# Kernel tuning notes

Hardware: AMD Instinct MI355X
Metric: run time of the kernel (lower is better)

## Reference

```python
import jax, jax.numpy as jnp
import numpy as np

B, S, D, H, F = 4, 1024, 1024, 16, 4096
DH = D // H
EPS = 1e-3  # keras LayerNormalization default epsilon


def _layer_norm(x, g, b):
    mu = jnp.mean(x, axis=-1, keepdims=True)
    var = jnp.mean(jnp.square(x - mu), axis=-1, keepdims=True)
    return (x - mu) * jax.lax.rsqrt(var + EPS) * g + b


def setup_inputs() -> dict:
    key = jax.random.key(0)
    ks = jax.random.split(key, 12)
    p = lambda k, shape: (0.02 * jax.random.normal(k, shape, dtype=jnp.float32))
    inp = {
        "inputs": jax.random.normal(ks[0], (B, S, D), dtype=jnp.float32),
        "paddings": jnp.zeros((B, S), dtype=jnp.float32),
        "attention_bias": jax.random.normal(ks[1], (B, H, S, S), dtype=jnp.float32),
        "attention_mask": jnp.ones((B, S, S), dtype=jnp.float32),
        "ln1_g": jnp.ones((D,), jnp.float32), "ln1_b": jnp.zeros((D,), jnp.float32),
        "wq": p(ks[2], (D, D)), "bq": jnp.zeros((D,), jnp.float32),
        "wk": p(ks[3], (D, D)), "bk": jnp.zeros((D,), jnp.float32),
        "wv": p(ks[4], (D, D)), "bv": jnp.zeros((D,), jnp.float32),
        "wo": p(ks[5], (D, D)), "bo": jnp.zeros((D,), jnp.float32),
        "ln2_g": jnp.ones((D,), jnp.float32), "ln2_b": jnp.zeros((D,), jnp.float32),
        "w1": p(ks[6], (D, F)), "b1": jnp.zeros((F,), jnp.float32),
        "w2": p(ks[7], (F, D)), "b2": jnp.zeros((D,), jnp.float32),
    }
    return inp


def reference(inputs, paddings, attention_bias, attention_mask,
              ln1_g, ln1_b, wq, bq, wk, bk, wv, bv, wo, bo,
              ln2_g, ln2_b, w1, b1, w2, b2):
    # ----- combined mask: [B,S,S] (broadcast over heads) -----
    keep = 1.0 - paddings                           # [B,S]
    pad_mask = keep[:, :, None] * keep[:, None, :]  # [B,T,S]
    mask = attention_mask * pad_mask                # [B,T,S]

    # ----- self-attention on pre-normalized inputs -----
    xn = _layer_norm(inputs, ln1_g, ln1_b)          # [B,S,D]
    q = (xn @ wq + bq).reshape(B, S, H, DH)
    k = (xn @ wk + bk).reshape(B, S, H, DH)
    v = (xn @ wv + bv).reshape(B, S, H, DH)

    logits = jnp.einsum('bthd,bshd->bhts', q, k) / jnp.sqrt(jnp.float32(DH))
    logits = logits + attention_bias - 1e9 * (1.0 - mask[:, None, :, :])
    attn = jax.nn.softmax(logits, axis=-1)          # [B,H,T,S]
    ctx = jnp.einsum('bhts,bshd->bthd', attn, v).reshape(B, S, D)
    atten_out = ctx @ wo + bo + inputs              # residual

    # ----- feed-forward block -----
    yn = _layer_norm(atten_out, ln2_g, ln2_b)
    h = jax.nn.gelu(yn @ w1 + b1, approximate=False)  # keras 'gelu' is exact
    out = atten_out + (h @ w2 + b2)
    out = out * (1.0 - paddings[:, :, None])
    return out
```

## Files before the change

kernel.cpp:

```cpp
#include <hip/hip_runtime.h>
#include <cstdint>
#include <cstddef>

#define B_   4
#define S_   1024
#define D_   1024
#define H_   16
#define DH_  64
#define F_   4096
#define MTOT 4096
#define QKV3 3072
#define KOFF 1024
#define VOFF 2048
#define SMBASE 16.0f

typedef __bf16 bf16x8 __attribute__((ext_vector_type(8)));
typedef float  f32x4  __attribute__((ext_vector_type(4)));

__device__ __forceinline__ unsigned short f2bf(float f){
  uint32_t u = __builtin_bit_cast(uint32_t, f);
  u += 0x7fffu + ((u >> 16) & 1u);
  return (unsigned short)(u >> 16);
}

__device__ __forceinline__ void gload_lds16(const void* g, void* l){
  __builtin_amdgcn_global_load_lds((__attribute__((address_space(1))) void*)(g),
                                   (__attribute__((address_space(3))) void*)(l),
                                   16, 0, 0);
}

__global__ __launch_bounds__(256) void prep_weights(const float* __restrict__ wq,
                                                    const float* __restrict__ wk,
                                                    const float* __restrict__ wv,
                                                    const float* __restrict__ wo,
                                                    const float* __restrict__ w1,
                                                    const float* __restrict__ w2,
                                                    const float* __restrict__ bq,
                                                    const float* __restrict__ bk,
                                                    const float* __restrict__ bv,
                                                    unsigned short* __restrict__ wqkvT,
                                                    unsigned short* __restrict__ woT,
                                                    unsigned short* __restrict__ w1T,
                                                    unsigned short* __restrict__ w2T,
                                                    float* __restrict__ bqkv){
  __shared__ float tile[32][33];
  const int bid = blockIdx.x;
  const int tx = threadIdx.x, ty = threadIdx.y;
  const float* W; unsigned short* WT; int K, N, n0, k0;
  if (bid < 3072){
    W  = (bid < 1024) ? wq : (bid < 2048) ? wk : wv;
    WT = wqkvT + (size_t)(bid >> 10) * D_ * D_;
    K = D_; N = D_;
    const int t = bid & 1023; n0 = (t & 31) * 32; k0 = (t >> 5) * 32;
  } else if (bid < 4096){
    W = wo; WT = woT; K = D_; N = D_;
    const int t = bid - 3072; n0 = (t & 31) * 32; k0 = (t >> 5) * 32;
  } else if (bid < 8192){
    W = w1; WT = w1T; K = D_; N = F_;
    const int t = bid - 4096; n0 = (t & 127) * 32; k0 = (t >> 7) * 32;
  } else {
    W = w2; WT = w2T; K = F_; N = D_;
    const int t = bid - 8192; n0 = (t & 31) * 32; k0 = (t >> 5) * 32;
  }
  #pragma unroll
  for (int i = 0; i < 4; ++i)
    tile[ty + i*8][tx] = W[(size_t)(k0 + ty + i*8) * N + n0 + tx];
  __syncthreads();
  #pragma unroll
  for (int i = 0; i < 4; ++i)
    WT[(size_t)(n0 + ty + i*8) * K + k0 + tx] = f2bf(tile[tx][ty + i*8]);
  if (bid < 12){
    const int i = bid*256 + ty*32 + tx;
    bqkv[i] = (i < 1024) ? bq[i] : (i < 2048) ? bk[i - 1024] : bv[i - 2048];
  }
}

__global__ __launch_bounds__(256) void mid_prep(const unsigned short* __restrict__ qkv,
                                                unsigned short* __restrict__ vt,
                                                const float* __restrict__ amask,
                                                const float* __restrict__ pad,
                                                float* __restrict__ madd){
  const int bid = blockIdx.x;
  if (bid < 4096){
    __shared__ unsigned short tile[32][33];
    const int tx = threadIdx.x, ty = threadIdx.y;
    const int s0 = (bid & 31) * 32;
    const int d0 = ((bid >> 5) & 1) * 32;
    const int bh = bid >> 6;
    const int b = bh >> 4, hh = bh & 15;
    #pragma unroll
    for (int i = 0; i < 4; ++i)
      tile[ty + i*8][tx] = qkv[(size_t)(b*S_ + s0 + ty + i*8) * QKV3 + VOFF + hh*DH_ + d0 + tx];
    __syncthreads();
    #pragma unroll
    for (int i = 0; i < 4; ++i)
      vt[((size_t)bh*DH_ + d0 + ty + i*8) * S_ + s0 + tx] = tile[tx][ty + i*8];
  } else {
    const int tid = threadIdx.y*32 + threadIdx.x;
    const int total = B_ * S_ * S_ / 4;
    for (int idx = (bid - 4096)*256 + tid; idx < total; idx += 2048*256){
      const int e0 = idx * 4;
      const int b = e0 >> 20;
      const int t = (e0 >> 10) & (S_ - 1);
      const int s = e0 & (S_ - 1);
      const float kt = 1.0f - pad[b*S_ + t];
      const float4 m = *(const float4*)(amask + e0);
      float4 o;
      o.x = -1e9f * (1.0f - m.x * kt * (1.0f - pad[b*S_ + s + 0]));
      o.y = -1e9f * (1.0f - m.y * kt * (1.0f - pad[b*S_ + s + 1]));
      o.z = -1e9f * (1.0f - m.z * kt * (1.0f - pad[b*S_ + s + 2]));
      o.w = -1e9f * (1.0f - m.w * kt * (1.0f - pad[b*S_ + s + 3]));
      *(float4*)(madd + e0) = o;
    }
  }
}

__global__ __launch_bounds__(256) void ln_kernel(const float* __restrict__ x,
                                                 const float* __restrict__ g,
                                                 const float* __restrict__ b,
                                                 unsigned short* __restrict__ out){
  const int row = blockIdx.x;
  const int tid = threadIdx.x;
  float4 xv = ((const float4*)(x + (size_t)row * D_))[tid];
  float s  = xv.x + xv.y + xv.z + xv.w;
  float s2 = xv.x*xv.x + xv.y*xv.y + xv.z*xv.z + xv.w*xv.w;
  #pragma unroll
  for (int off = 32; off > 0; off >>= 1){
    s  += __shfl_down(s, off);
    s2 += __shfl_down(s2, off);
  }
  __shared__ float ws1[4], ws2[4];
  const int w = tid >> 6, lane = tid & 63;
  if (lane == 0){ ws1[w] = s; ws2[w] = s2; }
  __syncthreads();
  const float tot  = ws1[0] + ws1[1] + ws1[2] + ws1[3];
  const float tot2 = ws2[0] + ws2[1] + ws2[2] + ws2[3];
  const float mean = tot * (1.0f / D_);
  const float var  = tot2 * (1.0f / D_) - mean * mean;
  const float rstd = rsqrtf(var + 1e-3f);
  const int c0 = tid * 4;
  ushort4 o;
  o.x = f2bf((xv.x - mean) * rstd * g[c0+0] + b[c0+0]);
  o.y = f2bf((xv.y - mean) * rstd * g[c0+1] + b[c0+1]);
  o.z = f2bf((xv.z - mean) * rstd * g[c0+2] + b[c0+2]);
  o.w = f2bf((xv.w - mean) * rstd * g[c0+3] + b[c0+3]);
  *(ushort4*)(out + (size_t)row * D_ + c0) = o;
}

template<int EPI, int BM>
__global__ __launch_bounds__(256) void gemm_bt(const unsigned short* __restrict__ A,
                                               const unsigned short* __restrict__ BT,
                                               const float* __restrict__ bias,
                                               const float* __restrict__ resid,
                                               const float* __restrict__ pad,
                                               unsigned short* __restrict__ outB,
                                               float* __restrict__ outF,
                                               int N, int K){
  constexpr int MR = BM / 32;
  constexpr int RA = BM / 32;
  __shared__ unsigned short As[BM * 64];
  __shared__ unsigned short Bs[128 * 64];
  const int tid  = threadIdx.x;
  const int lane = tid & 63, w = tid >> 6;
  const int wr = w >> 1, wc = w & 1;
  const int lm = lane & 15, l4 = lane >> 4;
  const int xsw = (lm & 7) << 3;
  const int m0 = blockIdx.x * BM, n0 = blockIdx.y * 128;

  const int rrow = tid >> 3;
  const int ce   = (((tid & 7) ^ (rrow & 7)) << 3);
  const unsigned short* Asrc = A  + (size_t)(m0 + rrow) * K + ce;
  const unsigned short* Bsrc = BT + (size_t)(n0 + rrow) * K + ce;

  f32x4 acc[MR][4] = {};

  #pragma unroll
  for (int ra = 0; ra < RA; ++ra)
    gload_lds16(Asrc + (size_t)(ra*32) * K, &As[(ra*256 + w*64) * 8]);
  #pragma unroll
  for (int rb = 0; rb < 4; ++rb)
    gload_lds16(Bsrc + (size_t)(rb*32) * K, &Bs[(rb*256 + w*64) * 8]);

  for (int k0 = 0; k0 < K; k0 += 64){
    __syncthreads();

    bf16x8 a[MR][2], bb[4][2];
    #pragma unroll
    for (int m = 0; m < MR; ++m)
      #pragma unroll
      for (int kc = 0; kc < 2; ++kc)
        a[m][kc] = *(const bf16x8*)&As[(wr*(BM/2) + m*16 + lm)*64 + ((kc*32 + l4*8) ^ xsw)];
    #pragma unroll
    for (int n = 0; n < 4; ++n)
      #pragma unroll
      for (int kc = 0; kc < 2; ++kc)
        bb[n][kc] = *(const bf16x8*)&Bs[(wc*64 + n*16 + lm)*64 + ((kc*32 + l4*8) ^ xsw)];

    __syncthreads();

    if (k0 + 64 < K){
      #pragma unroll
      for (int ra = 0; ra < RA; ++ra)
        gload_lds16(Asrc + (size_t)(ra*32) * K + (k0 + 64), &As[(ra*256 + w*64) * 8]);
      #pragma unroll
      for (int rb = 0; rb < 4; ++rb)
        gload_lds16(Bsrc + (size_t)(rb*32) * K + (k0 + 64), &Bs[(rb*256 + w*64) * 8]);
    }

    #pragma unroll
    for (int m = 0; m < MR; ++m)
      #pragma unroll
      for (int n = 0; n < 4; ++n)
        #pragma unroll
        for (int kc = 0; kc < 2; ++kc)
          acc[m][n] = __builtin_amdgcn_mfma_f32_16x16x32_bf16(a[m][kc], bb[n][kc], acc[m][n], 0, 0, 0);
  }

  #pragma unroll
  for (int m = 0; m < MR; ++m){
    #pragma unroll
    for (int n = 0; n < 4; ++n){
      #pragma unroll
      for (int r = 0; r < 4; ++r){
        const int row = m0 + wr*(BM/2) + m*16 + l4*4 + r;
        const int col = n0 + wc*64 + n*16 + lm;
        const size_t idx = (size_t)row * N + col;
        float vv = acc[m][n][r] + bias[col];
        if constexpr (EPI == 0){
          outB[idx] = f2bf(vv);
        } else if constexpr (EPI == 1){
          outF[idx] = vv + resid[idx];
        } else if constexpr (EPI == 2){
          outB[idx] = f2bf(0.5f * vv * (1.0f + erff(vv * 0.70710678118654752f)));
        } else {
          float t = vv + resid[idx];
          outF[idx] = t * (1.0f - pad[row]);
        }
      }
    }
  }
}

__global__ __launch_bounds__(256) void attn_kernel(const unsigned short* __restrict__ qkv,
                                                   const unsigned short* __restrict__ vt,
                                                   const float* __restrict__ abias,
                                                   const float* __restrict__ madd,
                                                   unsigned short* __restrict__ ctx){
  const int bid = blockIdx.x;
  const int id2 = (bid & 7) * 128 + (bid >> 3);
  const int tt = id2 & 15, h = (id2 >> 4) & 15, b = id2 >> 8;
  const int t0 = tt * 64;
  const int tid = threadIdx.x;
  const int lane = tid & 63, w = tid >> 6;
  const int lm = lane & 15, l4 = lane >> 4;
  const int xsw = (lm & 7) << 3;

  __shared__ unsigned short Ks[64 * 64];
  __shared__ unsigned short VTs[64 * 64];
  __shared__ unsigned short Ps[4][16 * 72];

  bf16x8 aq[2];
  {
    const int tg = t0 + w*16 + lm;
    const size_t qb = (size_t)(b*S_ + tg) * QKV3 + h*DH_;
    aq[0] = *(const bf16x8*)&qkv[qb + 0  + l4*8];
    aq[1] = *(const bf16x8*)&qkv[qb + 32 + l4*8];
  }

  const unsigned short* kbase = qkv + (size_t)(b*S_) * QKV3 + KOFF + h*DH_;
  const unsigned short* vbase = vt  + (size_t)((b*H_ + h) * DH_) * S_;
  const float* biasbase = abias + (size_t)((b*H_ + h) * S_ + t0 + w*16 + l4*4) * S_;
  const float* maddbase = madd  + (size_t)(b*S_ + t0 + w*16 + l4*4) * S_;

  const int r_st  = tid >> 3;
  const int ce_st = (((tid & 7) ^ (r_st & 7)) << 3);
  const unsigned short* kst = kbase + (size_t)r_st * QKV3 + ce_st;
  const unsigned short* vst = vbase + (size_t)r_st * S_ + ce_st;

  f32x4 accO[4] = {};
  float lrow[4] = {};
  float bmA[4][4], bmB[4][4];

  #pragma unroll
  for (int n = 0; n < 4; ++n){
    const int sg = n*16 + lm;
    #pragma unroll
    for (int r = 0; r < 4; ++r)
      bmA[n][r] = biasbase[(size_t)r * S_ + sg] + maddbase[(size_t)r * S_ + sg];
  }
  gload_lds16(kst,                   &Ks[w*512]);
  gload_lds16(kst + (size_t)32*QKV3, &Ks[2048 + w*512]);
  gload_lds16(vst,                   &VTs[w*512]);
  gload_lds16(vst + 32*S_,           &VTs[2048 + w*512]);

  auto step = [&](int s0, float (&cur)[4][4], float (&nxt)[4][4]){
    __syncthreads();

    const int sn = (s0 + 64 < S_) ? (s0 + 64) : s0;
    #pragma unroll
    for (int n = 0; n < 4; ++n){
      const int sg = sn + n*16 + lm;
      #pragma unroll
      for (int r = 0; r < 4; ++r)
        nxt[n][r] = biasbase[(size_t)r * S_ + sg] + maddbase[(size_t)r * S_ + sg];
    }

    f32x4 accS[4] = {};
    __builtin_amdgcn_s_setprio(1);
    #pragma unroll
    for (int n = 0; n < 4; ++n)
      #pragma unroll
      for (int kc = 0; kc < 2; ++kc){
        bf16x8 bk_ = *(const bf16x8*)&Ks[(n*16 + lm)*64 + ((kc*32 + l4*8) ^ xsw)];
        accS[n] = __builtin_amdgcn_mfma_f32_16x16x32_bf16(aq[kc], bk_, accS[n], 0, 0, 0);
      }
    __builtin_amdgcn_s_setprio(0);

    bf16x8 bvv[4][2];
    #pragma unroll
    for (int n = 0; n < 4; ++n)
      #pragma unroll
      for (int ks = 0; ks < 2; ++ks)
        bvv[n][ks] = *(const bf16x8*)&VTs[(n*16 + lm)*64 + ((ks*32 + l4*8) ^ xsw)];

    __syncthreads();

    if (s0 + 64 < S_){
      gload_lds16(kst + (size_t)(s0 + 64)*QKV3, &Ks[w*512]);
      gload_lds16(kst + (size_t)(s0 + 96)*QKV3, &Ks[2048 + w*512]);
      gload_lds16(vst + (s0 + 64),              &VTs[w*512]);
      gload_lds16(vst + 32*S_ + (s0 + 64),      &VTs[2048 + w*512]);
    }

    float ps[4] = {};
    #pragma unroll
    for (int n = 0; n < 4; ++n){
      #pragma unroll
      for (int r = 0; r < 4; ++r){
        const float pv = __expf(fmaf(accS[n][r], 0.125f, cur[n][r]) - SMBASE);
        accS[n][r] = pv;
        ps[r] += pv;
      }
    }
    #pragma unroll
    for (int r = 0; r < 4; ++r){
      float s = ps[r];
      s += __shfl_xor(s, 1); s += __shfl_xor(s, 2);
      s += __shfl_xor(s, 4); s += __shfl_xor(s, 8);
      lrow[r] += s;
    }

    #pragma unroll
    for (int n = 0; n < 4; ++n)
      #pragma unroll
      for (int r = 0; r < 4; ++r)
        Ps[w][(l4*4 + r)*72 + n*16 + lm] = f2bf(accS[n][r]);

    __builtin_amdgcn_s_setprio(1);
    #pragma unroll
    for (int ks = 0; ks < 2; ++ks){
      bf16x8 ap = *(const bf16x8*)&Ps[w][lm*72 + ks*32 + l4*8];
      #pragma unroll
      for (int n = 0; n < 4; ++n)
        accO[n] = __builtin_amdgcn_mfma_f32_16x16x32_bf16(ap, bvv[n][ks], accO[n], 0, 0, 0);
    }
    __builtin_amdgcn_s_setprio(0);
  };

  #pragma unroll 1
  for (int s0 = 0; s0 < S_; s0 += 128){
    step(s0,      bmA, bmB);
    step(s0 + 64, bmB, bmA);
  }

  #pragma unroll
  for (int n = 0; n < 4; ++n)
    #pragma unroll
    for (int r = 0; r < 4; ++r){
      const int tg = t0 + w*16 + l4*4 + r;
      ctx[(size_t)(b*S_ + tg) * D_ + h*DH_ + n*16 + lm] = f2bf(accO[n][r] / lrow[r]);
    }
}

extern "C" void kernel_launch(void* const* d_in, const int* in_sizes, int n_in,
                              void* d_out, int out_size, void* d_ws, size_t ws_size,
                              hipStream_t stream){
  (void)in_sizes; (void)n_in; (void)out_size; (void)ws_size;
  const float* x     = (const float*)d_in[0];
  const float* pad   = (const float*)d_in[1];
  const float* abias = (const float*)d_in[2];
  const float* amask = (const float*)d_in[3];
  const float* ln1g  = (const float*)d_in[4];
  const float* ln1b  = (const float*)d_in[5];
  const float* wq    = (const float*)d_in[6];
  const float* bq    = (const float*)d_in[7];
  const float* wk    = (const float*)d_in[8];
  const float* bk    = (const float*)d_in[9];
  const float* wv    = (const float*)d_in[10];
  const float* bv    = (const float*)d_in[11];
  const float* wo    = (const float*)d_in[12];
  const float* bo    = (const float*)d_in[13];
  const float* ln2g  = (const float*)d_in[14];
  const float* ln2b  = (const float*)d_in[15];
  const float* w1    = (const float*)d_in[16];
  const float* b1    = (const float*)d_in[17];
  const float* w2    = (const float*)d_in[18];
  const float* b2    = (const float*)d_in[19];
  float* out = (float*)d_out;

  char* p = (char*)d_ws;
  auto take = [&](size_t bytes){ void* r = (void*)p; p += bytes; return r; };
  unsigned short* xn   = (unsigned short*)take((size_t)MTOT * D_ * 2);
  unsigned short* qkv  = (unsigned short*)take((size_t)MTOT * QKV3 * 2);
  unsigned short* ctx  = (unsigned short*)take((size_t)MTOT * D_ * 2);
  unsigned short* yn   = (unsigned short*)take((size_t)MTOT * D_ * 2);
  unsigned short* hb   = (unsigned short*)take((size_t)MTOT * F_ * 2);
  float*          ao   = (float*)take((size_t)MTOT * D_ * 4);
  unsigned short* wqkvT= (unsigned short*)take((size_t)QKV3 * D_ * 2);
  unsigned short* woT  = (unsigned short*)take((size_t)D_ * D_ * 2);
  unsigned short* w1T  = (unsigned short*)take((size_t)D_ * F_ * 2);
  unsigned short* w2T  = (unsigned short*)take((size_t)D_ * F_ * 2);
  float*          bqkv = (float*)take((size_t)QKV3 * 4);
  unsigned short* vtb  = xn;
  float*          madd = (float*)hb;

  const dim3 tb(32, 8);

  prep_weights<<<12288, tb, 0, stream>>>(wq, wk, wv, wo, w1, w2, bq, bk, bv,
                                         wqkvT, woT, w1T, w2T, bqkv);

  ln_kernel<<<MTOT, 256, 0, stream>>>(x, ln1g, ln1b, xn);

  gemm_bt<0,128><<<dim3(MTOT/128, QKV3/128), 256, 0, stream>>>(xn, wqkvT, bqkv, nullptr, nullptr, qkv, nullptr, QKV3, D_);

  mid_prep<<<6144, tb, 0, stream>>>(qkv, vtb, amask, pad, madd);

  attn_kernel<<<dim3(16*H_*B_), 256, 0, stream>>>(qkv, vtb, abias, madd, ctx);

  gemm_bt<1,64><<<dim3(MTOT/64, D_/128), 256, 0, stream>>>(ctx, woT, bo, x, nullptr, nullptr, ao, D_, D_);

  ln_kernel<<<MTOT, 256, 0, stream>>>(ao, ln2g, ln2b, yn);

  gemm_bt<2,128><<<dim3(MTOT/128, F_/128), 256, 0, stream>>>(yn, w1T, b1, nullptr, nullptr, hb, nullptr, F_, D_);

  gemm_bt<3,64><<<dim3(MTOT/64, D_/128), 256, 0, stream>>>(hb, w2T, b2, ao, pad, nullptr, out, D_, F_);
}
```

Before: 304.7 us.

## Double-buffer K/V tiles in attention kernel and swizzle P scratch layout

The attention kernel now keeps two LDS buffers for K and V^T tiles. The next tile's async load is issued at the start of each step, so each iteration needs one barrier instead of two and V fragments are read straight from LDS at PV time rather than held in registers. The P scratch buffer drops its 72-element padded stride for a 64-wide XOR-swizzled layout to avoid bank conflicts with less LDS. This doubles K/V LDS use, which may lower occupancy. Correctness relies on the single barrier being enough to stop a buffer from being overwritten while another wave still reads it.

```diff
diff --git a/kernel.cpp b/kernel.cpp
--- a/kernel.cpp
+++ b/kernel.cpp
@@ -255,9 +255,9 @@
   const int lm = lane & 15, l4 = lane >> 4;
   const int xsw = (lm & 7) << 3;
 
-  __shared__ unsigned short Ks[64 * 64];
-  __shared__ unsigned short VTs[64 * 64];
-  __shared__ unsigned short Ps[4][16 * 72];
+  __shared__ unsigned short Ks[2][64 * 64];
+  __shared__ unsigned short VTs[2][64 * 64];
+  __shared__ unsigned short Ps[4][16 * 64];
 
   bf16x8 aq[2];
   {
@@ -281,6 +281,10 @@
   float lrow[4] = {};
   float bmA[4][4], bmB[4][4];
 
+  gload_lds16(kst,                   &Ks[0][w*512]);
+  gload_lds16(kst + (size_t)32*QKV3, &Ks[0][2048 + w*512]);
+  gload_lds16(vst,                   &VTs[0][w*512]);
+  gload_lds16(vst + 32*S_,           &VTs[0][2048 + w*512]);
   #pragma unroll
   for (int n = 0; n < 4; ++n){
     const int sg = n*16 + lm;
@@ -288,21 +292,23 @@
     for (int r = 0; r < 4; ++r)
       bmA[n][r] = biasbase[(size_t)r * S_ + sg] + maddbase[(size_t)r * S_ + sg];
   }
-  gload_lds16(kst,                   &Ks[w*512]);
-  gload_lds16(kst + (size_t)32*QKV3, &Ks[2048 + w*512]);
-  gload_lds16(vst,                   &VTs[w*512]);
-  gload_lds16(vst + 32*S_,           &VTs[2048 + w*512]);
-
-  auto step = [&](int s0, float (&cur)[4][4], float (&nxt)[4][4]){
+
+  auto step = [&](int s0, int buf, float (&cur)[4][4], float (&nxt)[4][4]){
     __syncthreads();
 
-    const int sn = (s0 + 64 < S_) ? (s0 + 64) : s0;
-    #pragma unroll
-    for (int n = 0; n < 4; ++n){
-      const int sg = sn + n*16 + lm;
-      #pragma unroll
-      for (int r = 0; r < 4; ++r)
-        nxt[n][r] = biasbase[(size_t)r * S_ + sg] + maddbase[(size_t)r * S_ + sg];
+    const int s1 = s0 + 64;
+    if (s1 < S_){
+      gload_lds16(kst + (size_t)s1*QKV3,        &Ks[buf^1][w*512]);
+      gload_lds16(kst + (size_t)(s1 + 32)*QKV3, &Ks[buf^1][2048 + w*512]);
+      gload_lds16(vst + s1,                     &VTs[buf^1][w*512]);
+      gload_lds16(vst + 32*S_ + s1,             &VTs[buf^1][2048 + w*512]);
+      #pragma unroll
+      for (int n = 0; n < 4; ++n){
+        const int sg = s1 + n*16 + lm;
+        #pragma unroll
+        for (int r = 0; r < 4; ++r)
+          nxt[n][r] = biasbase[(size_t)r * S_ + sg] + maddbase[(size_t)r * S_ + sg];
+      }
     }
 
     f32x4 accS[4] = {};
@@ -311,26 +317,10 @@
     for (int n = 0; n < 4; ++n)
       #pragma unroll
       for (int kc = 0; kc < 2; ++kc){
-        bf16x8 bk_ = *(const bf16x8*)&Ks[(n*16 + lm)*64 + ((kc*32 + l4*8) ^ xsw)];
+        bf16x8 bk_ = *(const bf16x8*)&Ks[buf][(n*16 + lm)*64 + ((kc*32 + l4*8) ^ xsw)];
         accS[n] = __builtin_amdgcn_mfma_f32_16x16x32_bf16(aq[kc], bk_, accS[n], 0, 0, 0);
       }
     __builtin_amdgcn_s_setprio(0);
-
-    bf16x8 bvv[4][2];
-    #pragma unroll
-    for (int n = 0; n < 4; ++n)
-      #pragma unroll
-      for (int ks = 0; ks < 2; ++ks)
-        bvv[n][ks] = *(const bf16x8*)&VTs[(n*16 + lm)*64 + ((ks*32 + l4*8) ^ xsw)];
-
-    __syncthreads();
-
-    if (s0 + 64 < S_){
-      gload_lds16(kst + (size_t)(s0 + 64)*QKV3, &Ks[w*512]);
-      gload_lds16(kst + (size_t)(s0 + 96)*QKV3, &Ks[2048 + w*512]);
-      gload_lds16(vst + (s0 + 64),              &VTs[w*512]);
-      gload_lds16(vst + 32*S_ + (s0 + 64),      &VTs[2048 + w*512]);
-    }
 
     float ps[4] = {};
     #pragma unroll
@@ -353,24 +343,28 @@
     #pragma unroll
     for (int n = 0; n < 4; ++n)
       #pragma unroll
-      for (int r = 0; r < 4; ++r)
-        Ps[w][(l4*4 + r)*72 + n*16 + lm] = f2bf(accS[n][r]);
+      for (int r = 0; r < 4; ++r){
+        const int prow = l4*4 + r;
+        Ps[w][prow*64 + ((n*16 + lm) ^ ((prow & 7) << 3))] = f2bf(accS[n][r]);
+      }
 
     __builtin_amdgcn_s_setprio(1);
     #pragma unroll
     for (int ks = 0; ks < 2; ++ks){
-      bf16x8 ap = *(const bf16x8*)&Ps[w][lm*72 + ks*32 + l4*8];
-      #pragma unroll
-      for (int n = 0; n < 4; ++n)
-        accO[n] = __builtin_amdgcn_mfma_f32_16x16x32_bf16(ap, bvv[n][ks], accO[n], 0, 0, 0);
+      bf16x8 ap = *(const bf16x8*)&Ps[w][lm*64 + ((ks*32 + l4*8) ^ xsw)];
+      #pragma unroll
+      for (int n = 0; n < 4; ++n){
+        bf16x8 bv_ = *(const bf16x8*)&VTs[buf][(n*16 + lm)*64 + ((ks*32 + l4*8) ^ xsw)];
+        accO[n] = __builtin_amdgcn_mfma_f32_16x16x32_bf16(ap, bv_, accO[n], 0, 0, 0);
+      }
     }
     __builtin_amdgcn_s_setprio(0);
   };
 
   #pragma unroll 1
   for (int s0 = 0; s0 < S_; s0 += 128){
-    step(s0,      bmA, bmB);
-    step(s0 + 64, bmB, bmA);
+    step(s0,      0, bmA, bmB);
+    step(s0 + 64, 1, bmB, bmA);
   }
 
   #pragma unroll
```

Result: no change. 309.8 us (+1.7%).
